# Kernel optimization log

Hardware: AMD Instinct MI355X
Metric: run time of the kernel (lower is better)

The kernel has to match this reference:

```python
import jax, jax.numpy as jnp
import numpy as np

B, N, E = 8, 4096, 65536
H, DH, GH = 4, 16, 64            # gat heads, head_dim, gat hidden
EDGE_EMBED = 16
D_FUSION = 640 + 64 + 640 + 40   # 1384


def setup_inputs() -> dict:
    key = jax.random.key(0)
    ks = jax.random.split(key, 24)
    rn = lambda i, shape, s=0.05: jax.random.normal(ks[i], shape, dtype=jnp.float32) * s
    return {
        'rnafm': rn(0, (B, 640), 1.0),
        'edit_delta': rn(1, (B, 640), 1.0),
        'hand_feat': rn(2, (B, 40), 1.0),
        'node_feats': rn(3, (B, N, 22), 1.0),
        'edge_index': jax.random.randint(ks[4], (B, 2, E), 0, N, dtype=jnp.int32),
        'edge_type': jax.random.randint(ks[5], (B, E), 0, 3, dtype=jnp.int32),
        'node_proj_w': rn(6, (GH, 22)), 'node_proj_b': jnp.zeros((GH,), jnp.float32),
        'gat_W': rn(7, (3, GH, GH)),
        'gat_a_src': rn(8, (3, H, DH)), 'gat_a_dst': rn(9, (3, H, DH)),
        'gat_a_edge': rn(10, (3, H, EDGE_EMBED)),
        'gat_edge_embed': rn(11, (3, 3, EDGE_EMBED)),
        'gat_ln_g': jnp.ones((3, GH), jnp.float32), 'gat_ln_b': jnp.zeros((3, GH), jnp.float32),
        'gat_out_w': rn(12, (64, GH)), 'gat_out_b': jnp.zeros((64,), jnp.float32),
        'enc1_w': rn(13, (256, D_FUSION)), 'enc1_b': jnp.zeros((256,), jnp.float32),
        'enc_ln_g': jnp.ones((256,), jnp.float32), 'enc_ln_b': jnp.zeros((256,), jnp.float32),
        'enc2_w': rn(14, (128, 256)), 'enc2_b': jnp.zeros((128,), jnp.float32),
        'bin_w': rn(15, (1, 128)), 'bin_b': jnp.zeros((1,), jnp.float32),
        'adp1_w': rn(16, (5, 32, 128)), 'adp1_b': jnp.zeros((5, 32), jnp.float32),
        'adp2_w': rn(17, (5, 1, 32)), 'adp2_b': jnp.zeros((5, 1), jnp.float32),
        'cls1_w': rn(18, (64, 128)), 'cls1_b': jnp.zeros((64,), jnp.float32),
        'cls2_w': rn(19, (6, 64)), 'cls2_b': jnp.zeros((6,), jnp.float32),
    }


def _layernorm(x, g, b, eps=1e-5):
    m = x.mean(-1, keepdims=True)
    v = ((x - m) ** 2).mean(-1, keepdims=True)
    return (x - m) / jnp.sqrt(v + eps) * g + b


def _gat_layer(x, src, dst, et, W, a_src, a_dst, a_edge, eemb, g, b):
    """x: [N, GH] -> [N, GH]; per-edge attention + scatter-softmax + scatter-add."""
    n = x.shape[0]
    h = x @ W.T                          # [N, GH]
    hh = h.reshape(n, H, DH)
    h_src, h_dst = hh[src], hh[dst]      # [E, H, DH] gathers
    attn = (jnp.einsum('ehd,hd->eh', h_src, a_src)
            + jnp.einsum('ehd,hd->eh', h_dst, a_dst)
            + eemb[et] @ a_edge.T)       # [E, H]
    attn = jnp.where(attn >= 0, attn, 0.2 * attn)  # leaky_relu(0.2)
    amax = jnp.maximum(jax.ops.segment_max(attn, dst, num_segments=n), -1e9)
    ex = jnp.exp(attn - amax[dst])
    denom = jax.ops.segment_sum(ex, dst, num_segments=n)
    an = ex / (denom[dst] + 1e-10)       # dropout is identity in eval
    agg = jax.ops.segment_sum(h_src * an[:, :, None], dst, num_segments=n)
    return _layernorm(agg.reshape(n, H * DH) + h, g, b)


def reference(rnafm, edit_delta, hand_feat, node_feats, edge_index, edge_type,
              node_proj_w, node_proj_b, gat_W, gat_a_src, gat_a_dst, gat_a_edge,
              gat_edge_embed, gat_ln_g, gat_ln_b, gat_out_w, gat_out_b,
              enc1_w, enc1_b, enc_ln_g, enc_ln_b, enc2_w, enc2_b,
              bin_w, bin_b, adp1_w, adp1_b, adp2_w, adp2_b,
              cls1_w, cls1_b, cls2_w, cls2_b):
    gelu = lambda t: jax.nn.gelu(t, approximate=False)

    def per_graph(nf, ei, et):
        x = nf @ node_proj_w.T + node_proj_b
        for l in range(3):
            x = gelu(_gat_layer(x, ei[0], ei[1], et, gat_W[l], gat_a_src[l],
                                gat_a_dst[l], gat_a_edge[l], gat_edge_embed[l],
                                gat_ln_g[l], gat_ln_b[l]))
        return x[x.shape[0] // 2]        # center node embedding

    gat_emb = jax.vmap(per_graph)(node_feats, edge_index, edge_type)   # [B, GH]
    gat_o = gat_emb @ gat_out_w.T + gat_out_b                          # [B, 64]
    fused = jnp.concatenate([rnafm, gat_o, edit_delta, hand_feat], axis=-1)
    h1 = _layernorm(gelu(fused @ enc1_w.T + enc1_b), enc_ln_g, enc_ln_b)
    shared = gelu(h1 @ enc2_w.T + enc2_b)                              # [B, 128]
    binary = (shared @ bin_w.T + bin_b)[:, 0]                          # [B]
    a1 = gelu(jnp.einsum('bf,hif->bhi', shared, adp1_w) + adp1_b)      # [B, 5, 32]
    per_enz = jnp.einsum('bhi,hi->bh', a1, adp2_w[:, 0, :]) + adp2_b[:, 0]  # [B, 5]
    cls = gelu(shared @ cls1_w.T + cls1_b) @ cls2_w.T + cls2_b         # [B, 6]
    return (binary, per_enz, cls, shared)
```

## Files before the change

### kernel.cpp

```cpp
#include <hip/hip_runtime.h>
#include <hip/hip_bf16.h>
#include <math.h>

#define BB 8
#define NN 4096
#define EE 65536
#define LOG2E 1.4426950408889634f

__device__ __forceinline__ float my_erf(float x){
  float ax = fabsf(x);
  float tt = 1.f/(1.f + 0.3275911f*ax);
  float poly = ((((1.061405429f*tt - 1.453152027f)*tt + 1.421413741f)*tt
                 - 0.284496736f)*tt + 0.254829592f)*tt;
  float y = 1.f - poly*expf(-ax*ax);
  return x >= 0.f ? y : -y;
}
__device__ __forceinline__ float gelu_f(float x){ return 0.5f*x*(1.0f + my_erf(x*0.7071067811865476f)); }
__device__ __forceinline__ float ld(const void* p, long i){ return ((const float*)p)[i]; }

__global__ __launch_bounds__(256) void k_pre(
    const void* __restrict__ nf, const void* __restrict__ pw, const void* __restrict__ pb,
    const void* __restrict__ W, const void* __restrict__ a_src, const void* __restrict__ a_dst,
    const void* __restrict__ a_edge, const void* __restrict__ eemb,
    const int* __restrict__ ei, const int* __restrict__ ety,
    float* __restrict__ h, float* __restrict__ sdot, float* __restrict__ ebt,
    int* __restrict__ cursor, int* __restrict__ csr, int b0, int nb, int NF){
  if ((int)blockIdx.x < NF){
    int fi = (int)blockIdx.x;
    int bpb = NF / nb;
    int b, q;
    if (nb == BB){ b = fi & 7; q = fi >> 3; }
    else         { b = fi / bpb; q = fi - b*bpb; }
    int e4 = q*256 + threadIdx.x;
    const int* base = ei + (long)(b0+b)*2*EE;
    int4 s4 = ((const int4*)base)[e4];
    int4 d4 = ((const int4*)(base + EE))[e4];
    int4 t4 = ((const int4*)(ety + (long)(b0+b)*EE))[e4];
    int* cb = cursor + b*NN;
    int ss[4] = {s4.x & (NN-1), s4.y & (NN-1), s4.z & (NN-1), s4.w & (NN-1)};
    int dd[4] = {d4.x & (NN-1), d4.y & (NN-1), d4.z & (NN-1), d4.w & (NN-1)};
    int tt[4] = {t4.x, t4.y, t4.z, t4.w};
    #pragma unroll
    for (int i=0;i<4;i++){
      int ty = tt[i]; ty = (ty < 0) ? 0 : (ty > 2 ? 2 : ty);
      int p = atomicAdd(&cb[dd[i]], 1);
      if (p < 64) csr[((long)(b*NN) + dd[i])*64 + p] = ss[i] | (ty << 12);
    }
    return;
  }

  __attribute__((aligned(16))) __shared__ float wlT[64*68];
  __attribute__((aligned(16))) __shared__ float nfl[32*24];
  __attribute__((aligned(16))) __shared__ float xs[32*68];
  int t = threadIdx.x;
  int lb = (int)blockIdx.x - NF;

  if (lb == 0 && t < 48){
    int ll = t >> 4, r = t & 15;
    if (r < 12){
      int ty = r >> 2, hd2 = r & 3;
      float s = 0.f;
      #pragma unroll
      for (int k=0;k<16;k++)
        s += ld(eemb, ll*48 + ty*16 + k) * ld(a_edge, ll*64 + hd2*16 + k);
      ebt[t] = s * LOG2E;
    }
  }
  {
    #pragma unroll
    for (int idx = t; idx < 1024; idx += 256){
      int row = idx >> 4, chunk = idx & 15;
      float4 wv = *((const float4*)((const float*)W + row*64 + chunk*4));
      *((float4*)&wlT[row*68 + chunk*4]) = wv;
    }
  }
  {
    long nfbase = ((long)b0*NN + (long)lb*32)*22;
    for (int idx = t; idx < 704; idx += 256){
      int row = idx / 22, k = idx - row*22;
      nfl[row*24 + k] = ld(nf, nfbase + idx);
    }
  }

  int w = t >> 6;
  int c = t & 63;
  int hd = c >> 4, dd = c & 15;
  long n0 = (long)lb*32 + w*8;

  float wreg[22];
  #pragma unroll
  for (int k = 0; k < 22; k++) wreg[k] = ld(pw, c*22 + k);
  float bias = ld(pb, c);
  __syncthreads();
  if (n0 >= nb*NN) return;

  #pragma unroll
  for (int i=0;i<8;i++){
    const float* nr = nfl + (w*8+i)*24;
    float a = bias;
    #pragma unroll
    for (int kc = 0; kc < 5; kc++){
      float4 nv = *((const float4*)&nr[kc*4]);
      a += nv.x*wreg[kc*4] + nv.y*wreg[kc*4+1] + nv.z*wreg[kc*4+2] + nv.w*wreg[kc*4+3];
    }
    a += nr[20]*wreg[20] + nr[21]*wreg[21];
    xs[(w*8+i)*68 + c] = a;
  }

  float acc[8] = {0.f,0.f,0.f,0.f,0.f,0.f,0.f,0.f};
  const float* xw = xs + (w*8)*68;
  const float* wr2 = wlT + c*68;
  #pragma unroll 4
  for (int kk=0;kk<16;kk++){
    float4 wv = *((const float4*)&wr2[kk*4]);
    #pragma unroll
    for (int i=0;i<8;i++){
      float4 xv = *((const float4*)&xw[i*68 + kk*4]);
      acc[i] += xv.x*wv.x + xv.y*wv.y + xv.z*wv.z + xv.w*wv.w;
    }
  }

  float cas = ld(a_src, c) * LOG2E;
  float cad = ld(a_dst, c) * LOG2E;
  #pragma unroll
  for (int i=0;i<8;i++){
    h[(n0+i)*64 + c] = acc[i];
    float ps = acc[i]*cas, pd = acc[i]*cad;
    #pragma unroll
    for (int o=8;o>=1;o>>=1){
      ps += __shfl_xor(ps,o,64);
      pd += __shfl_xor(pd,o,64);
    }
    if (dd == 0){
      sdot[(n0+i)*8 + hd]     = ps;
      sdot[(n0+i)*8 + 4 + hd] = pd;
    }
  }
}

__device__ __forceinline__ float gat_node(const float* __restrict__ hb,
    const float* __restrict__ sb, const int* __restrict__ cb, int dg,
    float sdP, float ebP0, float ebP1, float ebP2,
    float hdst, int c, int hd,
    const void* lng, const void* lnb, int l){
  int hL = c & 3;
  float denP = 0.f, acc = 0.f;
  int npass = (dg + 15) >> 4;
  for (int p = 0; p < npass; p++){
    int eidx = (p << 4) + (c >> 2);
    int pk = cb[eidx];
    int src = pk & 4095, ty = (pk >> 12) & 3;
    float av = sb[src*8 + hL] + sdP + (ty==0?ebP0:(ty==1?ebP1:ebP2));
    av = fmaxf(av, 0.2f*av);
    float ev = exp2f(av);
    if (eidx >= dg) ev = 0.f;
    denP += ev;
    int jmax = dg - (p << 4); if (jmax > 16) jmax = 16;
    #pragma unroll 4
    for (int j = 0; j < jmax; j++){
      float evj = __shfl(ev, j*4 + hd, 64);
      int sj = __builtin_amdgcn_readlane(pk, j*4) & 4095;
      acc += hb[(long)sj*64 + c] * evj;
    }
  }
  #pragma unroll
  for (int o=4;o<=32;o<<=1) denP += __shfl_xor(denP, o, 64);
  float den = __shfl(denP, hd, 64);
  float y = acc / (den + 1e-10f) + hdst;

  float s = y;
  #pragma unroll
  for (int o=32;o>=1;o>>=1) s += __shfl_xor(s, o, 64);
  float mean = s * (1.f/64.f);
  float d = y - mean;
  float vs = d*d;
  #pragma unroll
  for (int o=32;o>=1;o>>=1) vs += __shfl_xor(vs, o, 64);
  float var = vs * (1.f/64.f);
  float outv = d * rsqrtf(var + 1e-5f) * ld(lng, l*64+c) + ld(lnb, l*64+c);
  return gelu_f(outv);
}

__device__ __forceinline__ void gat_linear_tail(float g, float* xs, const float* wlT,
    const void* a_src, const void* a_dst, float* __restrict__ hOut,
    float* __restrict__ sdOut, long wave, int wloc, int c, int hd, int dd, int l){
  xs[wloc*68 + c] = g;
  float ha = 0.f;
  const float* xw = xs + wloc*68;
  const float* wr = wlT + c*68;
  #pragma unroll 4
  for (int kk=0;kk<16;kk++){
    float4 xv = *((const float4*)&xw[kk*4]);
    float4 wv = *((const float4*)&wr[kk*4]);
    ha += xv.x*wv.x + xv.y*wv.y + xv.z*wv.z + xv.w*wv.w;
  }
  hOut[wave*64 + c] = ha;
  float cas = ld(a_src, (long)(l+1)*64 + c) * LOG2E;
  float cad = ld(a_dst, (long)(l+1)*64 + c) * LOG2E;
  float ps = ha*cas, pd = ha*cad;
  #pragma unroll
  for (int o=8;o>=1;o>>=1){
    ps += __shfl_xor(ps,o,64);
    pd += __shfl_xor(pd,o,64);
  }
  if (dd == 0){
    sdOut[wave*8 + hd]     = ps;
    sdOut[wave*8 + 4 + hd] = pd;
  }
}

__global__ __launch_bounds__(256) void k_gatcone(
    const float* __restrict__ hIn, const float* __restrict__ sdIn,
    const float* __restrict__ ebt,
    const int* __restrict__ cursor, const int* __restrict__ csr,
    const void* __restrict__ lng, const void* __restrict__ lnb,
    const void* __restrict__ W,
    const void* __restrict__ a_src, const void* __restrict__ a_dst,
    float* __restrict__ hOut, float* __restrict__ sdOut,
    int l, int nb){
  __attribute__((aligned(16))) __shared__ float wlT[64*68];
  __attribute__((aligned(16))) __shared__ float xs[4*68];
  int t = threadIdx.x;
  int wloc = t >> 6;
  int b  = (int)blockIdx.x % nb;
  int ib = (int)blockIdx.x / nb;
  long wcen = (long)b*NN + NN/2;
  int dgc = cursor[wcen];
  dgc = (dgc < 0) ? 0 : (dgc > 64 ? 64 : dgc);
  int e0 = ib*4;
  if (e0/65 > dgc) return;
  {
    #pragma unroll
    for (int idx = t; idx < 1024; idx += 256){
      int row = idx >> 4, chunk = idx & 15;
      float4 wv = *((const float4*)((const float*)W + (long)(l+1)*4096 + row*64 + chunk*4));
      *((float4*)&wlT[row*68 + chunk*4]) = wv;
    }
  }
  __syncthreads();

  int e = e0 + wloc;
  int i = e / 65, j = e - i*65;
  long wave = -1;
  if (e < 4225 && i <= dgc){
    long vi = (i == 0) ? wcen : (long)b*NN + (csr[wcen*64 + (i-1)] & 4095);
    int dgi = cursor[vi];
    dgi = (dgi < 0) ? 0 : (dgi > 64 ? 64 : dgi);
    if (j == 0)            wave = vi;
    else if (j <= dgi)     wave = (long)b*NN + (csr[vi*64 + (j-1)] & 4095);
  }
  if (wave < 0) return;

  int c  = t & 63;
  int hd = c >> 4, dd = c & 15, hL = c & 3;

  float ebP0 = ebt[l*16 + 0 + hL];
  float ebP1 = ebt[l*16 + 4 + hL];
  float ebP2 = ebt[l*16 + 8 + hL];
  float sdP  = sdIn[wave*8 + 4 + hL];
  float hdst = hIn[wave*64 + c];
  int dg = __builtin_amdgcn_readfirstlane(cursor[wave]);
  dg = (dg < 0) ? 0 : (dg > 64 ? 64 : dg);
  const int* cb = csr + wave*64;
  const float* hb = hIn + (long)b*NN*64;
  const float* sb = sdIn + (long)b*NN*8;

  float g = gat_node(hb, sb, cb, dg, sdP, ebP0, ebP1, ebP2, hdst, c, hd, lng, lnb, l);
  gat_linear_tail(g, xs, wlT, a_src, a_dst, hOut, sdOut, wave, wloc, c, hd, dd, l);
}

__global__ __launch_bounds__(256) void k_gatlin2(
    const float* __restrict__ hIn, const float* __restrict__ sdIn,
    const float* __restrict__ ebt,
    const int* __restrict__ cursor, const int* __restrict__ csr,
    const void* __restrict__ lng, const void* __restrict__ lnb,
    const void* __restrict__ W,
    const void* __restrict__ a_src, const void* __restrict__ a_dst,
    float* __restrict__ hOut, float* __restrict__ sdOut,
    int l, int nb){
  __attribute__((aligned(16))) __shared__ float wlT[64*68];
  __attribute__((aligned(16))) __shared__ float xs[4*68];
  int t = threadIdx.x;
  {
    #pragma unroll
    for (int idx = t; idx < 1024; idx += 256){
      int row = idx >> 4, chunk = idx & 15;
      float4 wv = *((const float4*)((const float*)W + (long)(l+1)*4096 + row*64 + chunk*4));
      *((float4*)&wlT[row*68 + chunk*4]) = wv;
    }
  }
  __syncthreads();

  int wloc = t >> 6;
  int b  = (int)blockIdx.x % nb;
  int ib = (int)blockIdx.x / nb;
  int e  = ib*4 + wloc;
  long wcen = (long)b*NN + NN/2;
  int dgc = cursor[wcen];
  dgc = (dgc < 0) ? 0 : (dgc > 64 ? 64 : dgc);
  long wave;
  if (e == 0)            wave = wcen;
  else if (e <= dgc)     wave = (long)b*NN + (csr[wcen*64 + (e-1)] & 4095);
  else                   return;

  int c  = t & 63;
  int hd = c >> 4, dd = c & 15, hL = c & 3;

  float ebP0 = ebt[l*16 + 0 + hL];
  float ebP1 = ebt[l*16 + 4 + hL];
  float ebP2 = ebt[l*16 + 8 + hL];
  float sdP  = sdIn[wave*8 + 4 + hL];
  float hdst = hIn[wave*64 + c];
  int dg = __builtin_amdgcn_readfirstlane(cursor[wave]);
  dg = (dg < 0) ? 0 : (dg > 64 ? 64 : dg);
  const int* cb = csr + wave*64;
  const float* hb = hIn + (long)b*NN*64;
  const float* sb = sdIn + (long)b*NN*8;

  float g = gat_node(hb, sb, cb, dg, sdP, ebP0, ebP1, ebP2, hdst, c, hd, lng, lnb, l);
  gat_linear_tail(g, xs, wlT, a_src, a_dst, hOut, sdOut, wave, wloc, c, hd, dd, l);
}

__global__ __launch_bounds__(64) void k_gatfin(
    const float* __restrict__ hIn, const float* __restrict__ sdIn,
    const float* __restrict__ ebt,
    const int* __restrict__ cursor, const int* __restrict__ csr,
    const void* __restrict__ lng, const void* __restrict__ lnb,
    float* __restrict__ cemb, int l, int b0, int nb){
  int b = (int)blockIdx.x;
  if (b >= nb) return;
  long wave = (long)b*NN + NN/2;
  int c  = threadIdx.x & 63;
  int hd = c >> 4, hL = c & 3;

  float ebP0 = ebt[l*16 + 0 + hL];
  float ebP1 = ebt[l*16 + 4 + hL];
  float ebP2 = ebt[l*16 + 8 + hL];
  float sdP  = sdIn[wave*8 + 4 + hL];
  float hdst = hIn[wave*64 + c];
  int dg = __builtin_amdgcn_readfirstlane(cursor[wave]);
  dg = (dg < 0) ? 0 : (dg > 64 ? 64 : dg);
  const int* cb = csr + wave*64;
  const float* hb = hIn + (long)b*NN*64;
  const float* sb = sdIn + (long)b*NN*8;
  cemb[(b0+b)*64 + c] = gat_node(hb, sb, cb, dg, sdP, ebP0, ebP1, ebP2, hdst, c, hd, lng, lnb, l);
}

__global__ __launch_bounds__(256) void k_enc1(const float* __restrict__ ctr,
    const void* rnafm, const void* edelta, const void* hand,
    const void* gow, const void* gob,
    const void* e1w, const void* e1b, float* __restrict__ g1){
  __shared__ float fb[1384];
  __shared__ float femb[64];
  int b = blockIdx.x, t = threadIdx.x;
  for (int i=t;i<640;i+=256){
    fb[i]     = ld(rnafm,  b*640+i);
    fb[704+i] = ld(edelta, b*640+i);
  }
  if (t<40) fb[1344+t] = ld(hand, b*40+t);
  if (t>=64 && t<128){
    int cc = t-64;
    femb[cc] = ctr[b*64+cc];
  }
  __syncthreads();
  if (t<64){
    float acc = ld(gob, t);
    #pragma unroll 8
    for (int k=0;k<64;k++) acc += femb[k]*ld(gow, t*64+k);
    fb[640+t] = acc;
  }
  __syncthreads();
  int w = t >> 6, lane = t & 63;
  int c = blockIdx.y*4 + w;
  long wr = (long)c*1384;
  float acc = 0.f;
  #pragma unroll 7
  for (int i=0;i<21;i++){
    int k = lane + 64*i;
    acc += fb[k]*ld(e1w, wr+k);
  }
  if (lane < 40){
    int k = 1344+lane;
    acc += fb[k]*ld(e1w, wr+k);
  }
  #pragma unroll
  for (int o=32;o>=1;o>>=1) acc += __shfl_xor(acc, o, 64);
  if (lane==0) g1[b*256+c] = gelu_f(acc + ld(e1b, c));
}

__global__ __launch_bounds__(256) void k_enc2(const float* __restrict__ g1,
    const void* lng, const void* lnb, const void* e2w, const void* e2b,
    float* __restrict__ shs, float* __restrict__ out){
  __shared__ float red[256];
  __shared__ float h1s[256];
  int b = blockIdx.x, t = threadIdx.x;
  float g = g1[b*256+t];
  red[t] = g; __syncthreads();
  for (int s=128;s>=1;s>>=1){ if (t<s) red[t]+=red[t+s]; __syncthreads(); }
  float mean = red[0]*(1.f/256.f); __syncthreads();
  red[t] = (g-mean)*(g-mean); __syncthreads();
  for (int s=128;s>=1;s>>=1){ if (t<s) red[t]+=red[t+s]; __syncthreads(); }
  float var = red[0]*(1.f/256.f);
  h1s[t] = (g-mean)*rsqrtf(var+1e-5f)*ld(lng, t) + ld(lnb, t);
  __syncthreads();
  int w = t >> 6, lane = t & 63;
  int c = blockIdx.y*4 + w;
  long wr = (long)c*256;
  float acc = 0.f;
  #pragma unroll
  for (int i=0;i<4;i++){
    int k = lane + 64*i;
    acc += h1s[k]*ld(e2w, wr+k);
  }
  #pragma unroll
  for (int o=32;o>=1;o>>=1) acc += __shfl_xor(acc, o, 64);
  if (lane==0){
    float s = gelu_f(acc + ld(e2b, c));
    shs[b*128+c] = s;
    out[96 + b*128 + c] = s;
  }
}

__global__ __launch_bounds__(256) void k_mid(const float* __restrict__ shs,
    const void* a1w, const void* a1b, const void* c1w, const void* c1b,
    float* __restrict__ a1s, float* __restrict__ c1s){
  int b = blockIdx.x;
  int w = threadIdx.x >> 6, lane = threadIdx.x & 63;
  int idx = blockIdx.y*4 + w;
  const float* sb = shs + b*128;
  if (idx < 160){
    long wr = (long)idx*128;
    float acc = sb[lane]*ld(a1w, wr+lane) + sb[lane+64]*ld(a1w, wr+lane+64);
    #pragma unroll
    for (int o=32;o>=1;o>>=1) acc += __shfl_xor(acc, o, 64);
    if (lane==0) a1s[b*160+idx] = gelu_f(acc + ld(a1b, idx));
  } else {
    int c = idx - 160;
    long wr = (long)c*128;
    float acc = sb[lane]*ld(c1w, wr+lane) + sb[lane+64]*ld(c1w, wr+lane+64);
    #pragma unroll
    for (int o=32;o>=1;o>>=1) acc += __shfl_xor(acc, o, 64);
    if (lane==0) c1s[b*64+c] = gelu_f(acc + ld(c1b, c));
  }
}

__global__ __launch_bounds__(64) void k_fin(const float* __restrict__ shs,
    const float* __restrict__ a1s, const float* __restrict__ c1s,
    const void* binw, const void* binb, const void* a2w, const void* a2b,
    const void* c2w, const void* c2b,
    float* __restrict__ out){
  int b = blockIdx.x, t = threadIdx.x;
  {
    float p = shs[b*128+t]*ld(binw, t) + shs[b*128+t+64]*ld(binw, t+64);
    #pragma unroll
    for (int o=32;o>=1;o>>=1) p += __shfl_xor(p, o, 64);
    if (t==0) out[b] = p + ld(binb, 0);
  }
  if (t<5){
    float acc = ld(a2b, t);
    for (int i=0;i<32;i++) acc += a1s[b*160 + t*32+i]*ld(a2w, t*32+i);
    out[8 + b*5 + t] = acc;
  }
  if (t>=8 && t<14){
    int o = t-8;
    float acc = ld(c2b, o);
    for (int j=0;j<64;j++) acc += c1s[b*64+j]*ld(c2w, o*64+j);
    out[48 + b*6 + o] = acc;
  }
}

extern "C" void kernel_launch(void* const* d_in, const int* in_sizes, int n_in,
                              void* d_out, int out_size, void* d_ws, size_t ws_size,
                              hipStream_t stream) {
  const int* ei  = (const int*)d_in[4];
  const int* ety = (const int*)d_in[5];

  size_t need_full = 2048 + 512
                   + (size_t)4*((size_t)BB*NN)
                   + (size_t)4*((size_t)BB*NN*64)
                   + (size_t)4*3*((size_t)BB*NN*64)
                   + (size_t)4*2*((size_t)BB*NN*8)
                   + (size_t)4*(8*256 + 8*128 + 8*160 + 8*64 + 64);
  int nb = (ws_size >= need_full + (1u<<20)) ? BB : 1;

  char* ws = (char*)d_ws;
  float* cemb   = (float*)ws;
  float* ebt    = (float*)(ws + 2048 + 256);
  int*   cursor = (int*)(ws + 2048 + 512);
  int*   csr    = cursor + (size_t)nb*NN;
  float* hA     = (float*)(csr + (size_t)nb*NN*64);
  float* hB     = hA + (size_t)nb*NN*64;
  float* x      = hB + (size_t)nb*NN*64;
  float* sdotA  = x + (size_t)nb*NN*64;
  float* sdotB  = sdotA + (size_t)nb*NN*8;
  float* g1     = sdotB + (size_t)nb*NN*8;
  float* shs    = g1 + 8*256;
  float* a1s    = shs + 8*128;
  float* c1s    = a1s + 8*160;

  for (int b0 = 0; b0 < BB; b0 += nb){
    hipMemsetAsync(cursor, 0, (size_t)nb*NN*sizeof(int), stream);
    int NL = nb*NN/32;
    int NF = nb*(EE/1024);
    hipLaunchKernelGGL(k_pre, dim3(NF+NL), dim3(256), 0, stream,
                       d_in[3], d_in[6], d_in[7],
                       d_in[8], d_in[9], d_in[10], d_in[11], d_in[12],
                       ei, ety, hA, sdotA, ebt, cursor, csr, b0, nb, NF);
    hipLaunchKernelGGL(k_gatcone, dim3(nb*1057), dim3(256), 0, stream,
                       hA, sdotA, ebt, cursor, csr, d_in[13], d_in[14],
                       d_in[8], d_in[9], d_in[10], hB, sdotB, 0, nb);
    hipLaunchKernelGGL(k_gatlin2, dim3(nb*17), dim3(256), 0, stream,
                       hB, sdotB, ebt, cursor, csr, d_in[13], d_in[14],
                       d_in[8], d_in[9], d_in[10], hA, sdotA, 1, nb);
    hipLaunchKernelGGL(k_gatfin, dim3(nb), dim3(64), 0, stream,
                       hA, sdotA, ebt, cursor, csr, d_in[13], d_in[14],
                       cemb, 2, b0, nb);
  }

  hipLaunchKernelGGL(k_enc1, dim3(BB, 64), dim3(256), 0, stream,
                     cemb,
                     d_in[0], d_in[1], d_in[2], d_in[15], d_in[16],
                     d_in[17], d_in[18], g1);
  hipLaunchKernelGGL(k_enc2, dim3(BB, 32), dim3(256), 0, stream,
                     g1, d_in[19], d_in[20], d_in[21], d_in[22], shs, (float*)d_out);
  hipLaunchKernelGGL(k_mid,  dim3(BB, 56), dim3(256), 0, stream,
                     shs, d_in[25], d_in[26], d_in[29], d_in[30], a1s, c1s);
  hipLaunchKernelGGL(k_fin,  dim3(BB), dim3(64), 0, stream,
                     shs, a1s, c1s, d_in[23], d_in[24], d_in[27], d_in[28],
                     d_in[31], d_in[32], (float*)d_out);
}
```

Before: 211.9 us.

## Fuse GAT layers 2-3 into one block, pack CSR as u16, fold final head

```diff
diff --git a/kernel.cpp b/kernel.cpp
--- a/kernel.cpp
+++ b/kernel.cpp
@@ -24,7 +24,7 @@
     const void* __restrict__ a_edge, const void* __restrict__ eemb,
     const int* __restrict__ ei, const int* __restrict__ ety,
     float* __restrict__ h, float* __restrict__ sdot, float* __restrict__ ebt,
-    int* __restrict__ cursor, int* __restrict__ csr, int b0, int nb, int NF){
+    int* __restrict__ cursor, unsigned short* __restrict__ csr, int b0, int nb, int NF){
   if ((int)blockIdx.x < NF){
     int fi = (int)blockIdx.x;
     int bpb = NF / nb;
@@ -44,7 +44,7 @@
     for (int i=0;i<4;i++){
       int ty = tt[i]; ty = (ty < 0) ? 0 : (ty > 2 ? 2 : ty);
       int p = atomicAdd(&cb[dd[i]], 1);
-      if (p < 64) csr[((long)(b*NN) + dd[i])*64 + p] = ss[i] | (ty << 12);
+      if (p < 64) csr[((long)(b*NN) + dd[i])*64 + p] = (unsigned short)(ss[i] | (ty << 12));
     }
     return;
   }
@@ -139,7 +139,7 @@
 }
 
 __device__ __forceinline__ float gat_node(const float* __restrict__ hb,
-    const float* __restrict__ sb, const int* __restrict__ cb, int dg,
+    const float* __restrict__ sb, const unsigned short* __restrict__ cb, int dg,
     float sdP, float ebP0, float ebP1, float ebP2,
     float hdst, int c, int hd,
     const void* lng, const void* lnb, int l){
@@ -212,7 +212,7 @@
 __global__ __launch_bounds__(256) void k_gatcone(
     const float* __restrict__ hIn, const float* __restrict__ sdIn,
     const float* __restrict__ ebt,
-    const int* __restrict__ cursor, const int* __restrict__ csr,
+    const int* __restrict__ cursor, const unsigned short* __restrict__ csr,
     const void* __restrict__ lng, const void* __restrict__ lnb,
     const void* __restrict__ W,
     const void* __restrict__ a_src, const void* __restrict__ a_dst,
@@ -261,7 +261,7 @@
   float hdst = hIn[wave*64 + c];
   int dg = __builtin_amdgcn_readfirstlane(cursor[wave]);
   dg = (dg < 0) ? 0 : (dg > 64 ? 64 : dg);
-  const int* cb = csr + wave*64;
+  const unsigned short* cb = csr + wave*64;
   const float* hb = hIn + (long)b*NN*64;
   const float* sb = sdIn + (long)b*NN*8;
 
@@ -269,81 +269,113 @@
   gat_linear_tail(g, xs, wlT, a_src, a_dst, hOut, sdOut, wave, wloc, c, hd, dd, l);
 }
 
-__global__ __launch_bounds__(256) void k_gatlin2(
+__global__ __launch_bounds__(1024) void k_gat23(
     const float* __restrict__ hIn, const float* __restrict__ sdIn,
     const float* __restrict__ ebt,
-    const int* __restrict__ cursor, const int* __restrict__ csr,
+    const int* __restrict__ cursor, const unsigned short* __restrict__ csr,
     const void* __restrict__ lng, const void* __restrict__ lnb,
     const void* __restrict__ W,
     const void* __restrict__ a_src, const void* __restrict__ a_dst,
-    float* __restrict__ hOut, float* __restrict__ sdOut,
-    int l, int nb){
+    float* __restrict__ cemb, int b0, int nb){
   __attribute__((aligned(16))) __shared__ float wlT[64*68];
-  __attribute__((aligned(16))) __shared__ float xs[4*68];
+  __attribute__((aligned(16))) __shared__ float xsL[16*68];
+  __attribute__((aligned(16))) __shared__ float h2L[65*68];
+  __shared__ float sd2L[65*9];
   int t = threadIdx.x;
+  int b = (int)blockIdx.x;
+  if (b >= nb) return;
   {
-    #pragma unroll
-    for (int idx = t; idx < 1024; idx += 256){
-      int row = idx >> 4, chunk = idx & 15;
-      float4 wv = *((const float4*)((const float*)W + (long)(l+1)*4096 + row*64 + chunk*4));
-      *((float4*)&wlT[row*68 + chunk*4]) = wv;
-    }
-  }
-  __syncthreads();
-
-  int wloc = t >> 6;
-  int b  = (int)blockIdx.x % nb;
-  int ib = (int)blockIdx.x / nb;
-  int e  = ib*4 + wloc;
+    int row = t >> 4, chunk = t & 15;
+    float4 wv = *((const float4*)((const float*)W + 2*4096 + row*64 + chunk*4));
+    *((float4*)&wlT[row*68 + chunk*4]) = wv;
+  }
   long wcen = (long)b*NN + NN/2;
   int dgc = cursor[wcen];
   dgc = (dgc < 0) ? 0 : (dgc > 64 ? 64 : dgc);
-  long wave;
-  if (e == 0)            wave = wcen;
-  else if (e <= dgc)     wave = (long)b*NN + (csr[wcen*64 + (e-1)] & 4095);
-  else                   return;
-
-  int c  = t & 63;
+  int wv = t >> 6, c = t & 63;
   int hd = c >> 4, dd = c & 15, hL = c & 3;
-
-  float ebP0 = ebt[l*16 + 0 + hL];
-  float ebP1 = ebt[l*16 + 4 + hL];
-  float ebP2 = ebt[l*16 + 8 + hL];
-  float sdP  = sdIn[wave*8 + 4 + hL];
-  float hdst = hIn[wave*64 + c];
-  int dg = __builtin_amdgcn_readfirstlane(cursor[wave]);
-  dg = (dg < 0) ? 0 : (dg > 64 ? 64 : dg);
-  const int* cb = csr + wave*64;
   const float* hb = hIn + (long)b*NN*64;
   const float* sb = sdIn + (long)b*NN*8;
-
-  float g = gat_node(hb, sb, cb, dg, sdP, ebP0, ebP1, ebP2, hdst, c, hd, lng, lnb, l);
-  gat_linear_tail(g, xs, wlT, a_src, a_dst, hOut, sdOut, wave, wloc, c, hd, dd, l);
-}
-
-__global__ __launch_bounds__(64) void k_gatfin(
-    const float* __restrict__ hIn, const float* __restrict__ sdIn,
-    const float* __restrict__ ebt,
-    const int* __restrict__ cursor, const int* __restrict__ csr,
-    const void* __restrict__ lng, const void* __restrict__ lnb,
-    float* __restrict__ cemb, int l, int b0, int nb){
-  int b = (int)blockIdx.x;
-  if (b >= nb) return;
-  long wave = (long)b*NN + NN/2;
-  int c  = threadIdx.x & 63;
-  int hd = c >> 4, hL = c & 3;
-
-  float ebP0 = ebt[l*16 + 0 + hL];
-  float ebP1 = ebt[l*16 + 4 + hL];
-  float ebP2 = ebt[l*16 + 8 + hL];
-  float sdP  = sdIn[wave*8 + 4 + hL];
-  float hdst = hIn[wave*64 + c];
-  int dg = __builtin_amdgcn_readfirstlane(cursor[wave]);
-  dg = (dg < 0) ? 0 : (dg > 64 ? 64 : dg);
-  const int* cb = csr + wave*64;
-  const float* hb = hIn + (long)b*NN*64;
-  const float* sb = sdIn + (long)b*NN*8;
-  cemb[(b0+b)*64 + c] = gat_node(hb, sb, cb, dg, sdP, ebP0, ebP1, ebP2, hdst, c, hd, lng, lnb, l);
+  float eb10 = ebt[16 + 0 + hL], eb11 = ebt[16 + 4 + hL], eb12 = ebt[16 + 8 + hL];
+  float cas2 = ld(a_src, 2*64 + c) * LOG2E;
+  float cad2 = ld(a_dst, 2*64 + c) * LOG2E;
+  __syncthreads();
+
+  for (int r = 0; r < 5; r++){
+    int e = r*16 + wv;
+    if (e < 65 && e <= dgc){
+      long wave = (e == 0) ? wcen : (long)b*NN + (csr[wcen*64 + (e-1)] & 4095);
+      float sdP  = sdIn[wave*8 + 4 + hL];
+      float hdst = hIn[wave*64 + c];
+      int dg = __builtin_amdgcn_readfirstlane(cursor[wave]);
+      dg = (dg < 0) ? 0 : (dg > 64 ? 64 : dg);
+      const unsigned short* cb = csr + wave*64;
+      float g = gat_node(hb, sb, cb, dg, sdP, eb10, eb11, eb12, hdst, c, hd, lng, lnb, 1);
+      xsL[wv*68 + c] = g;
+      float ha = 0.f;
+      const float* xw = xsL + wv*68;
+      const float* wr = wlT + c*68;
+      #pragma unroll 4
+      for (int kk=0;kk<16;kk++){
+        float4 xv = *((const float4*)&xw[kk*4]);
+        float4 wvv = *((const float4*)&wr[kk*4]);
+        ha += xv.x*wvv.x + xv.y*wvv.y + xv.z*wvv.z + xv.w*wvv.w;
+      }
+      h2L[e*68 + c] = ha;
+      float ps = ha*cas2, pd = ha*cad2;
+      #pragma unroll
+      for (int o=8;o>=1;o>>=1){
+        ps += __shfl_xor(ps,o,64);
+        pd += __shfl_xor(pd,o,64);
+      }
+      if (dd == 0){
+        sd2L[e*9 + hd]     = ps;
+        sd2L[e*9 + 4 + hd] = pd;
+      }
+    }
+  }
+  __syncthreads();
+
+  if (t < 64){
+    float eb0 = ebt[32 + 0 + hL], eb1 = ebt[32 + 4 + hL], eb2 = ebt[32 + 8 + hL];
+    float sdP  = sd2L[4 + hL];
+    float hdst = h2L[c];
+    int dg = dgc;
+    const unsigned short* cb = csr + wcen*64;
+    float denP = 0.f, acc = 0.f;
+    int npass = (dg + 15) >> 4;
+    for (int p = 0; p < npass; p++){
+      int eidx = (p << 4) + (c >> 2);
+      int pk = cb[eidx];
+      int ty = (pk >> 12) & 3;
+      float av = sd2L[(eidx+1)*9 + hL] + sdP + (ty==0?eb0:(ty==1?eb1:eb2));
+      av = fmaxf(av, 0.2f*av);
+      float ev = exp2f(av);
+      if (eidx >= dg) ev = 0.f;
+      denP += ev;
+      int jmax = dg - (p << 4); if (jmax > 16) jmax = 16;
+      #pragma unroll 4
+      for (int j = 0; j < jmax; j++){
+        float evj = __shfl(ev, j*4 + hd, 64);
+        acc += h2L[(p*16 + j + 1)*68 + c] * evj;
+      }
+    }
+    #pragma unroll
+    for (int o=4;o<=32;o<<=1) denP += __shfl_xor(denP, o, 64);
+    float den = __shfl(denP, hd, 64);
+    float y = acc / (den + 1e-10f) + hdst;
+    float s = y;
+    #pragma unroll
+    for (int o=32;o>=1;o>>=1) s += __shfl_xor(s, o, 64);
+    float mean = s * (1.f/64.f);
+    float d = y - mean;
+    float vs = d*d;
+    #pragma unroll
+    for (int o=32;o>=1;o>>=1) vs += __shfl_xor(vs, o, 64);
+    float var = vs * (1.f/64.f);
+    float outv = d * rsqrtf(var + 1e-5f) * ld(lng, 2*64+c) + ld(lnb, 2*64+c);
+    cemb[(b0+b)*64 + c] = gelu_f(outv);
+  }
 }
 
 __global__ __launch_bounds__(256) void k_enc1(const float* __restrict__ ctr,
@@ -421,9 +453,12 @@
   }
 }
 
-__global__ __launch_bounds__(256) void k_mid(const float* __restrict__ shs,
+__global__ __launch_bounds__(256) void k_midfin(const float* __restrict__ shs,
     const void* a1w, const void* a1b, const void* c1w, const void* c1b,
-    float* __restrict__ a1s, float* __restrict__ c1s){
+    const void* binw, const void* binb, const void* a2w, const void* a2b,
+    const void* c2w, const void* c2b,
+    float* __restrict__ a1s, float* __restrict__ c1s,
+    int* __restrict__ ticket, float* __restrict__ out){
   int b = blockIdx.x;
   int w = threadIdx.x >> 6, lane = threadIdx.x & 63;
   int idx = blockIdx.y*4 + w;
@@ -442,30 +477,31 @@
     for (int o=32;o>=1;o>>=1) acc += __shfl_xor(acc, o, 64);
     if (lane==0) c1s[b*64+c] = gelu_f(acc + ld(c1b, c));
   }
-}
-
-__global__ __launch_bounds__(64) void k_fin(const float* __restrict__ shs,
-    const float* __restrict__ a1s, const float* __restrict__ c1s,
-    const void* binw, const void* binb, const void* a2w, const void* a2b,
-    const void* c2w, const void* c2b,
-    float* __restrict__ out){
-  int b = blockIdx.x, t = threadIdx.x;
-  {
-    float p = shs[b*128+t]*ld(binw, t) + shs[b*128+t+64]*ld(binw, t+64);
-    #pragma unroll
-    for (int o=32;o>=1;o>>=1) p += __shfl_xor(p, o, 64);
-    if (t==0) out[b] = p + ld(binb, 0);
-  }
-  if (t<5){
-    float acc = ld(a2b, t);
-    for (int i=0;i<32;i++) acc += a1s[b*160 + t*32+i]*ld(a2w, t*32+i);
-    out[8 + b*5 + t] = acc;
-  }
-  if (t>=8 && t<14){
-    int o = t-8;
-    float acc = ld(c2b, o);
-    for (int j=0;j<64;j++) acc += c1s[b*64+j]*ld(c2w, o*64+j);
-    out[48 + b*6 + o] = acc;
+  __threadfence();
+  __shared__ int lastf;
+  if (threadIdx.x == 0) lastf = (atomicAdd(&ticket[b], 1) == 55);
+  __syncthreads();
+  if (!lastf) return;
+  __threadfence();
+  int t = threadIdx.x;
+  if (t < 64){
+    {
+      float p = sb[t]*ld(binw, t) + sb[t+64]*ld(binw, t+64);
+      #pragma unroll
+      for (int o=32;o>=1;o>>=1) p += __shfl_xor(p, o, 64);
+      if (t==0) out[b] = p + ld(binb, 0);
+    }
+    if (t<5){
+      float acc = ld(a2b, t);
+      for (int i=0;i<32;i++) acc += a1s[b*160 + t*32+i]*ld(a2w, t*32+i);
+      out[8 + b*5 + t] = acc;
+    }
+    if (t>=8 && t<14){
+      int o = t-8;
+      float acc = ld(c2b, o);
+      for (int j=0;j<64;j++) acc += c1s[b*64+j]*ld(c2w, o*64+j);
+      out[48 + b*6 + o] = acc;
+    }
   }
 }
 
@@ -484,22 +520,22 @@
   int nb = (ws_size >= need_full + (1u<<20)) ? BB : 1;
 
   char* ws = (char*)d_ws;
-  float* cemb   = (float*)ws;
-  float* ebt    = (float*)(ws + 2048 + 256);
-  int*   cursor = (int*)(ws + 2048 + 512);
-  int*   csr    = cursor + (size_t)nb*NN;
-  float* hA     = (float*)(csr + (size_t)nb*NN*64);
-  float* hB     = hA + (size_t)nb*NN*64;
-  float* x      = hB + (size_t)nb*NN*64;
-  float* sdotA  = x + (size_t)nb*NN*64;
-  float* sdotB  = sdotA + (size_t)nb*NN*8;
-  float* g1     = sdotB + (size_t)nb*NN*8;
-  float* shs    = g1 + 8*256;
-  float* a1s    = shs + 8*128;
-  float* c1s    = a1s + 8*160;
+  float* cemb    = (float*)ws;
+  float* ebt     = (float*)(ws + 2048 + 256);
+  int*   cursor  = (int*)(ws + 2048 + 512);
+  int*   ticket  = cursor + (size_t)nb*NN;
+  unsigned short* csr = (unsigned short*)(ticket + 64);
+  float* hA      = (float*)((char*)csr + (size_t)nb*NN*64*2);
+  float* hB      = hA + (size_t)nb*NN*64;
+  float* sdotA   = hB + (size_t)nb*NN*64;
+  float* sdotB   = sdotA + (size_t)nb*NN*8;
+  float* g1      = sdotB + (size_t)nb*NN*8;
+  float* shs     = g1 + 8*256;
+  float* a1s     = shs + 8*128;
+  float* c1s     = a1s + 8*160;
 
   for (int b0 = 0; b0 < BB; b0 += nb){
-    hipMemsetAsync(cursor, 0, (size_t)nb*NN*sizeof(int), stream);
+    hipMemsetAsync(cursor, 0, ((size_t)nb*NN + 64)*sizeof(int), stream);
     int NL = nb*NN/32;
     int NF = nb*(EE/1024);
     hipLaunchKernelGGL(k_pre, dim3(NF+NL), dim3(256), 0, stream,
@@ -509,12 +545,9 @@
     hipLaunchKernelGGL(k_gatcone, dim3(nb*1057), dim3(256), 0, stream,
                        hA, sdotA, ebt, cursor, csr, d_in[13], d_in[14],
                        d_in[8], d_in[9], d_in[10], hB, sdotB, 0, nb);
-    hipLaunchKernelGGL(k_gatlin2, dim3(nb*17), dim3(256), 0, stream,
+    hipLaunchKernelGGL(k_gat23, dim3(nb), dim3(1024), 0, stream,
                        hB, sdotB, ebt, cursor, csr, d_in[13], d_in[14],
-                       d_in[8], d_in[9], d_in[10], hA, sdotA, 1, nb);
-    hipLaunchKernelGGL(k_gatfin, dim3(nb), dim3(64), 0, stream,
-                       hA, sdotA, ebt, cursor, csr, d_in[13], d_in[14],
-                       cemb, 2, b0, nb);
+                       d_in[8], d_in[9], d_in[10], cemb, b0, nb);
   }
 
   hipLaunchKernelGGL(k_enc1, dim3(BB, 64), dim3(256), 0, stream,
@@ -523,9 +556,8 @@
                      d_in[17], d_in[18], g1);
   hipLaunchKernelGGL(k_enc2, dim3(BB, 32), dim3(256), 0, stream,
                      g1, d_in[19], d_in[20], d_in[21], d_in[22], shs, (float*)d_out);
-  hipLaunchKernelGGL(k_mid,  dim3(BB, 56), dim3(256), 0, stream,
-                     shs, d_in[25], d_in[26], d_in[29], d_in[30], a1s, c1s);
-  hipLaunchKernelGGL(k_fin,  dim3(BB), dim3(64), 0, stream,
-                     shs, a1s, c1s, d_in[23], d_in[24], d_in[27], d_in[28],
-                     d_in[31], d_in[32], (float*)d_out);
-}
+  hipLaunchKernelGGL(k_midfin, dim3(BB, 56), dim3(256), 0, stream,
+                     shs, d_in[25], d_in[26], d_in[29], d_in[30],
+                     d_in[23], d_in[24], d_in[27], d_in[28], d_in[31], d_in[32],
+                     a1s, c1s, ticket, (float*)d_out);
+}
```

Result: slower. 249.0 us (+17.5%).
